# Performance work log

Hardware: AMD Instinct MI355X
Metric: run time of the kernel (lower is better)

Reference implementation:

```python
import jax, jax.numpy as jnp
import numpy as np

NR_HEADS = 8


def segment_softmax(scores, indices, num_segments):
    # numerically stable softmax within each segment
    seg_max = jax.ops.segment_max(scores, indices, num_segments=num_segments)
    e = jnp.exp(scores - seg_max[indices])
    denom = jax.ops.segment_sum(e, indices, num_segments=num_segments)
    return e / denom[indices]


def setup_inputs() -> dict:
    key = jax.random.key(0)
    ks = jax.random.split(key, 10)
    n_ast, d, n_cfg = 500000, 128, 32768
    H, combined = NR_HEADS, 128
    w_scale = 1.0 / np.sqrt(d)
    return {
        "ast_nodes_encodings": jax.random.normal(ks[0], (n_ast, d), jnp.float32),
        "Wq": jax.random.normal(ks[1], (H, d, d), jnp.float32) * w_scale,
        "bq": jnp.zeros((H, d), jnp.float32),
        "Wk": jax.random.normal(ks[2], (H, d, d), jnp.float32) * w_scale,
        "bk": jnp.zeros((H, d), jnp.float32),
        "Wo": jax.random.normal(ks[3], (H * d, combined), jnp.float32) * (1.0 / np.sqrt(H * d)),
        "bo": jnp.zeros((combined,), jnp.float32),
        "ast_key": jax.random.randint(ks[4], (n_ast,), 0, n_ast, jnp.int32),
        "ast_value": jax.random.randint(ks[5], (n_ast,), 0, n_cfg, jnp.int32),
        "pdg_key": jnp.arange(n_cfg, dtype=jnp.int32),
        "pdg_value": jax.random.randint(ks[6], (n_cfg,), 0, n_ast, jnp.int32),
        "nr_cfg_nodes": n_cfg,
    }


def reference(ast_nodes_encodings, Wq, bq, Wk, bk, Wo, bo,
              ast_key, ast_value, pdg_key, pdg_value, nr_cfg_nodes):
    N = int(nr_cfg_nodes)
    d = ast_nodes_encodings.shape[1]
    inv_sqrt_d = 1.0 / np.sqrt(d)

    # Build per-PDG-node attention queries: gather sub-AST root encodings, scatter into [N, d]
    root_encodings = ast_nodes_encodings[pdg_value]                   # [N_map, d]
    attn_queries = jnp.zeros((N, d), ast_nodes_encodings.dtype).at[pdg_key].set(root_encodings)

    # Gather scattered inputs (one row per AST node assigned to a PDG node)
    values = ast_nodes_encodings[ast_key]                              # [E, d]
    indices = ast_value                                                # [E]

    # Multi-head scatter attention (ScatterCombiner with combining_method='attn')
    head_outs = []
    for h in range(NR_HEADS):  # small fixed head count; avoids [E, H, d] intermediates
        q = attn_queries @ Wq[h] + bq[h]                               # [N, d]
        k = values @ Wk[h] + bk[h]                                     # [E, d]
        scores = jnp.sum(q[indices] * k, axis=-1) * inv_sqrt_d         # [E]
        probs = segment_softmax(scores, indices, N)                    # [E]
        head_outs.append(jax.ops.segment_sum(probs[:, None] * values, indices, num_segments=N))

    combined = jnp.concatenate(head_outs, axis=-1) @ Wo + bo           # [N, combined_dim]
    return combined
```

## Files before the change

kernel.cpp:

```cpp
#include <hip/hip_runtime.h>
#include <hip/hip_bf16.h>
#include <cstdint>

typedef __hip_bfloat16 bf16;
typedef unsigned int uint;
typedef unsigned short ushort;

#define DEVI __device__ __forceinline__

DEVI float blo(uint u){ return __uint_as_float(u << 16); }
DEVI float bhi(uint u){ return __uint_as_float(u & 0xffff0000u); }
DEVI ushort f2b(float x){ uint u = __float_as_uint(x); uint r = (u + 0x7fffu + ((u >> 16) & 1u)) >> 16; return (ushort)r; }
DEVI uint pack2(float a, float b){ return (uint)f2b(a) | ((uint)f2b(b) << 16); }
DEVI float b2f(ushort h){ return __uint_as_float((uint)h << 16); }

typedef short bf16x8 __attribute__((ext_vector_type(8)));
typedef float f32x4  __attribute__((ext_vector_type(4)));

__global__ __launch_bounds__(256) void build_M(const float* __restrict__ Wq, const float* __restrict__ Wk,
                                               float* __restrict__ Mb){
  __shared__ float WkL[128*33];
  __shared__ float WqL[16*33];
  const int t = threadIdx.x;
  const int h = blockIdx.x >> 3, pg = blockIdx.x & 7, p0 = pg*16;
  const float* wk = Wk + (size_t)h*16384;
  const float* wq = Wq + ((size_t)h*128 + p0)*128;
  const int m = t & 127, half = t >> 7;
  float acc[8] = {0,0,0,0,0,0,0,0};
  for (int jc = 0; jc < 4; ++jc){
    __syncthreads();
    #pragma unroll
    for (int i = 0; i < 4; ++i){
      int g = t + 256*i;
      int mm = g >> 3, j0 = (g & 7)*4;
      float4 v = *(const float4*)(wk + mm*128 + jc*32 + j0);
      float* d = &WkL[mm*33 + j0];
      d[0] = v.x; d[1] = v.y; d[2] = v.z; d[3] = v.w;
    }
    {
      int e = t*2;
      int pr = e >> 5, jj = e & 31;
      float2 v = *(const float2*)(wq + pr*128 + jc*32 + jj);
      WqL[pr*33 + jj] = v.x; WqL[pr*33 + jj + 1] = v.y;
    }
    __syncthreads();
    for (int j = 0; j < 32; ++j){
      float wkv = WkL[m*33 + j];
      #pragma unroll
      for (int r = 0; r < 8; ++r)
        acc[r] = fmaf(WqL[(half*8 + r)*33 + j], wkv, acc[r]);
    }
  }
  #pragma unroll
  for (int r = 0; r < 8; ++r)
    Mb[(size_t)(p0 + half*8 + r)*1024 + h*128 + m] = acc[r];
}

__global__ void build_bias(const float* __restrict__ Wq, const float* __restrict__ Wk,
                           const float* __restrict__ bq, const float* __restrict__ bk,
                           float* __restrict__ cvec, float* __restrict__ uvec, float* __restrict__ sv){
  int h = blockIdx.x, m = threadIdx.x;
  const float* wkr = Wk + ((size_t)h*128 + m)*128;
  const float* wqr = Wq + ((size_t)h*128 + m)*128;
  const float* bqr = bq + h*128;
  const float* bkr = bk + h*128;
  float c = 0.f, u = 0.f;
  for (int j = 0; j < 128; ++j){
    c = fmaf(wkr[j], bqr[j], c);
    u = fmaf(wqr[j], bkr[j], u);
  }
  cvec[h*128 + m] = c;
  uvec[h*128 + m] = u;
  if (m == 0){
    float s = 0.f;
    for (int j = 0; j < 128; ++j) s = fmaf(bqr[j], bkr[j], s);
    sv[h] = s;
  }
}

__global__ void scatter_aq(const int* __restrict__ pk, const int* __restrict__ pv,
                           const float* __restrict__ ast, float* __restrict__ aq, int n_map){
  int i = blockIdx.x;
  if (i >= n_map) return;
  int k = pk[i], src = pv[i];
  int lane = threadIdx.x;
  float2 v = *(const float2*)(ast + (size_t)src*128 + 2*lane);
  *(float2*)(aq + (size_t)k*128 + 2*lane) = v;
}

__global__ __launch_bounds__(256) void qt_gemm(const float* __restrict__ aq, const float* __restrict__ Mb,
                                               const float* __restrict__ cvec, bf16* __restrict__ qt, int N){
  __shared__ float aqL[32*128];
  const int t = threadIdx.x;
  const int n0 = blockIdx.x * 32;
  #pragma unroll
  for (int i = 0; i < 4; ++i){
    int f4 = t + 256*i;
    int r = f4 >> 5, p0 = (f4 & 31)*4;
    int row = n0 + r; if (row >= N) row = N - 1;
    *(float4*)(aqL + r*128 + p0) = *(const float4*)(aq + (size_t)row*128 + p0);
  }
  __syncthreads();
  const int cg = t & 63, rg = t >> 6;
  for (int chunk = 0; chunk < 4; ++chunk){
    const int c0 = chunk*256 + cg*4;
    float4 acc[8];
    #pragma unroll
    for (int r = 0; r < 8; ++r) acc[r] = make_float4(0.f,0.f,0.f,0.f);
    for (int p = 0; p < 128; ++p){
      float4 b4 = *(const float4*)(Mb + (size_t)p*1024 + c0);
      #pragma unroll
      for (int r = 0; r < 8; ++r){
        float a = aqL[(rg*8 + r)*128 + p];
        acc[r].x = fmaf(a, b4.x, acc[r].x);
        acc[r].y = fmaf(a, b4.y, acc[r].y);
        acc[r].z = fmaf(a, b4.z, acc[r].z);
        acc[r].w = fmaf(a, b4.w, acc[r].w);
      }
    }
    float4 cv = *(const float4*)(cvec + c0);
    #pragma unroll
    for (int r = 0; r < 8; ++r){
      int row = n0 + rg*8 + r;
      if (row < N){
        uint2 o;
        o.x = pack2(acc[r].x + cv.x, acc[r].y + cv.y);
        o.y = pack2(acc[r].z + cv.z, acc[r].w + cv.w);
        *(uint2*)(qt + (size_t)row*1024 + c0) = o;
      }
    }
  }
}

__global__ void qb_kernel(const float* __restrict__ aq, const float* __restrict__ uvec,
                          const float* __restrict__ sv, float* __restrict__ qb){
  int n = blockIdx.x, lane = threadIdx.x;
  int h = lane >> 3, g = lane & 7;
  const float* ar = aq + (size_t)n*128 + g*16;
  const float* ur = uvec + h*128 + g*16;
  float dot = 0.f;
  #pragma unroll
  for (int k = 0; k < 16; ++k) dot = fmaf(ar[k], ur[k], dot);
  dot += __shfl_xor(dot, 1);
  dot += __shfl_xor(dot, 2);
  dot += __shfl_xor(dot, 4);
  if (g == 0) qb[(size_t)n*8 + h] = dot + sv[h];
}

__global__ void count_edges(const int* __restrict__ av, int* __restrict__ counts, int E){
  int e = blockIdx.x*256 + threadIdx.x;
  if (e < E) atomicAdd(&counts[av[e]], 1);
}

__global__ void scan_offsets(const int* __restrict__ counts, int* __restrict__ offsets, int N){
  __shared__ int pa[1024];
  __shared__ int pb[1024];
  int t = threadIdx.x;
  int CH = (N + 1023) >> 10;
  int b = t*CH, e = b + CH;
  if (b > N) b = N;
  if (e > N) e = N;
  int s = 0;
  for (int i = b; i < e; ++i) s += counts[i];
  pa[t] = s;
  __syncthreads();
  int* src = pa; int* dst = pb;
  for (int off = 1; off < 1024; off <<= 1){
    int v = src[t];
    if (t >= off) v += src[t - off];
    __syncthreads();
    dst[t] = v;
    __syncthreads();
    int* tmp = src; src = dst; dst = tmp;
  }
  int run = src[t] - s;
  for (int i = b; i < e; ++i){ offsets[i] = run; run += counts[i]; }
  if (t == 1023) offsets[N] = src[1023];
}

__global__ void fill_edges(const int* __restrict__ av, const int* __restrict__ akey,
                           const int* __restrict__ offsets, int* __restrict__ cursor,
                           int* __restrict__ ridx, int E){
  int e = blockIdx.x*256 + threadIdx.x;
  if (e < E){
    int seg = av[e];
    int pos = offsets[seg] + atomicAdd(&cursor[seg], 1);
    ridx[pos] = akey[e];
  }
}

__global__ __launch_bounds__(256) void seg_attn(
    const bf16* __restrict__ qt, const float* __restrict__ qb,
    const int* __restrict__ offsets, const int* __restrict__ ridx,
    const float* __restrict__ ast, bf16* __restrict__ ho, int N)
{
  const int wid  = threadIdx.x >> 6;
  const int lane = threadIdx.x & 63;
  const int n = blockIdx.x*4 + wid;
  if (n >= N) return;
  const int beg = offsets[n];
  const int deg = offsets[n+1] - beg;
  const int h = lane >> 3, g = lane & 7;

  const uint4* qp = (const uint4*)(qt + (size_t)n*1024 + h*128 + g*16);
  const uint4 qa = qp[0], qc = qp[1];
  const float4 q0 = make_float4(blo(qa.x), bhi(qa.x), blo(qa.y), bhi(qa.y));
  const float4 q1 = make_float4(blo(qa.z), bhi(qa.z), blo(qa.w), bhi(qa.w));
  const float4 q2 = make_float4(blo(qc.x), bhi(qc.x), blo(qc.y), bhi(qc.y));
  const float4 q3 = make_float4(blo(qc.z), bhi(qc.z), blo(qc.w), bhi(qc.w));
  const float qbv = qb[(size_t)n*8 + h];
  const float isd = 0.08838834764831845f;

  float den = 0.f;
  float4 x0 = make_float4(0,0,0,0), x1 = x0, x2 = x0, x3 = x0;

  float4 vA = make_float4(0,0,0,0), vB = vA, vC = vA, vD = vA;
  if (deg > 0){
    const float4* vp = (const float4*)(ast + (size_t)ridx[beg]*128 + g*16);
    vA = vp[0]; vB = vp[1]; vC = vp[2]; vD = vp[3];
  }
  for (int e = 0; e < deg; ++e){
    const float4 a0 = vA, a1 = vB, a2 = vC, a3 = vD;
    const int e2 = (e + 1 < deg) ? (e + 1) : e;
    const float4* vpn = (const float4*)(ast + (size_t)ridx[beg + e2]*128 + g*16);
    vA = vpn[0]; vB = vpn[1]; vC = vpn[2]; vD = vpn[3];

    float dot = 0.f;
    dot = fmaf(a0.x, q0.x, dot); dot = fmaf(a0.y, q0.y, dot);
    dot = fmaf(a0.z, q0.z, dot); dot = fmaf(a0.w, q0.w, dot);
    dot = fmaf(a1.x, q1.x, dot); dot = fmaf(a1.y, q1.y, dot);
    dot = fmaf(a1.z, q1.z, dot); dot = fmaf(a1.w, q1.w, dot);
    dot = fmaf(a2.x, q2.x, dot); dot = fmaf(a2.y, q2.y, dot);
    dot = fmaf(a2.z, q2.z, dot); dot = fmaf(a2.w, q2.w, dot);
    dot = fmaf(a3.x, q3.x, dot); dot = fmaf(a3.y, q3.y, dot);
    dot = fmaf(a3.z, q3.z, dot); dot = fmaf(a3.w, q3.w, dot);
    dot += __shfl_xor(dot, 1);
    dot += __shfl_xor(dot, 2);
    dot += __shfl_xor(dot, 4);

    const float p = __expf((dot + qbv) * isd);
    den += p;
    x0.x = fmaf(p, a0.x, x0.x); x0.y = fmaf(p, a0.y, x0.y);
    x0.z = fmaf(p, a0.z, x0.z); x0.w = fmaf(p, a0.w, x0.w);
    x1.x = fmaf(p, a1.x, x1.x); x1.y = fmaf(p, a1.y, x1.y);
    x1.z = fmaf(p, a1.z, x1.z); x1.w = fmaf(p, a1.w, x1.w);
    x2.x = fmaf(p, a2.x, x2.x); x2.y = fmaf(p, a2.y, x2.y);
    x2.z = fmaf(p, a2.z, x2.z); x2.w = fmaf(p, a2.w, x2.w);
    x3.x = fmaf(p, a3.x, x3.x); x3.y = fmaf(p, a3.y, x3.y);
    x3.z = fmaf(p, a3.z, x3.z); x3.w = fmaf(p, a3.w, x3.w);
  }
  const float r = (deg > 0) ? (1.f / den) : 0.f;

  uint4 o0, o1;
  o0.x = pack2(x0.x*r, x0.y*r); o0.y = pack2(x0.z*r, x0.w*r);
  o0.z = pack2(x1.x*r, x1.y*r); o0.w = pack2(x1.z*r, x1.w*r);
  o1.x = pack2(x2.x*r, x2.y*r); o1.y = pack2(x2.z*r, x2.w*r);
  o1.z = pack2(x3.x*r, x3.y*r); o1.w = pack2(x3.z*r, x3.w*r);
  uint4* hb = (uint4*)(ho + (size_t)n*1024 + h*128 + g*16);
  hb[0] = o0;
  hb[1] = o1;
}

__global__ void wo_pack(const float* __restrict__ Wo, uint4* __restrict__ Wp){
  const int b = blockIdx.x;
  const int ks = b >> 3, ct = b & 7;
  const int l = threadIdx.x;
  const int kb = ks*32 + (l >> 4)*8;
  const int c  = ct*16 + (l & 15);
  ushort hi[8], lo[8];
  #pragma unroll
  for (int j = 0; j < 8; ++j){
    float wv = Wo[(size_t)(kb + j)*128 + c];
    ushort hh = f2b(wv);
    hi[j] = hh;
    lo[j] = f2b(wv - b2f(hh));
  }
  uint4 H, L;
  H.x = (uint)hi[0] | ((uint)hi[1] << 16);
  H.y = (uint)hi[2] | ((uint)hi[3] << 16);
  H.z = (uint)hi[4] | ((uint)hi[5] << 16);
  H.w = (uint)hi[6] | ((uint)hi[7] << 16);
  L.x = (uint)lo[0] | ((uint)lo[1] << 16);
  L.y = (uint)lo[2] | ((uint)lo[3] << 16);
  L.z = (uint)lo[4] | ((uint)lo[5] << 16);
  L.w = (uint)lo[6] | ((uint)lo[7] << 16);
  Wp[((size_t)b*2 + 0)*64 + l] = H;
  Wp[((size_t)b*2 + 1)*64 + l] = L;
}

__global__ __launch_bounds__(256, 1) void out_mfma(const bf16* __restrict__ ho, const uint4* __restrict__ Wp,
                                                   const float* __restrict__ bo, float* __restrict__ out, int N){
  const int l = threadIdx.x & 63, w = threadIdx.x >> 6;
  const int lr = l & 15, lk = l >> 4;
  const int r0 = blockIdx.x*128 + w*32;
  int ra = r0 + lr;      if (ra > N-1) ra = N-1;
  int rb = r0 + 16 + lr; if (rb > N-1) rb = N-1;
  const bf16* pa = ho + (size_t)ra*1024 + lk*8;
  const bf16* pb = ho + (size_t)rb*1024 + lk*8;
  const uint4* pw = Wp + l;

  f32x4 acc[2][8];
  #pragma unroll
  for (int i = 0; i < 2; ++i)
    #pragma unroll
    for (int c = 0; c < 8; ++c)
      #pragma unroll
      for (int j = 0; j < 4; ++j) acc[i][c][j] = 0.f;

  bf16x8 Aa[2], Ab[2], Ba[16], Bb[16];

  auto LD = [&](int ks, bf16x8* A, bf16x8* B){
    A[0] = *(const bf16x8*)(pa + ks*32);
    A[1] = *(const bf16x8*)(pb + ks*32);
    const uint4* q = pw + (size_t)ks*1024;
    #pragma unroll
    for (int u = 0; u < 16; ++u) B[u] = *(const bf16x8*)(q + (size_t)u*64);
  };
  auto MM = [&](bf16x8* A, bf16x8* B){
    #pragma unroll
    for (int c = 0; c < 8; ++c){
      acc[0][c] = __builtin_amdgcn_mfma_f32_16x16x32_bf16(A[0], B[2*c],   acc[0][c], 0, 0, 0);
      acc[1][c] = __builtin_amdgcn_mfma_f32_16x16x32_bf16(A[1], B[2*c],   acc[1][c], 0, 0, 0);
      acc[0][c] = __builtin_amdgcn_mfma_f32_16x16x32_bf16(A[0], B[2*c+1], acc[0][c], 0, 0, 0);
      acc[1][c] = __builtin_amdgcn_mfma_f32_16x16x32_bf16(A[1], B[2*c+1], acc[1][c], 0, 0, 0);
    }
  };

  LD(0, Aa, Ba);
  for (int ks = 0; ks < 32; ks += 2){
    LD(ks + 1, Ab, Bb);
    MM(Aa, Ba);
    if (ks + 2 < 32) LD(ks + 2, Aa, Ba);
    MM(Ab, Bb);
  }

  #pragma unroll
  for (int c = 0; c < 8; ++c){
    float bv = bo[c*16 + lr];
    #pragma unroll
    for (int rt = 0; rt < 2; ++rt){
      #pragma unroll
      for (int i = 0; i < 4; ++i){
        int rr = r0 + rt*16 + lk*4 + i;
        if (rr < N) out[(size_t)rr*128 + c*16 + lr] = acc[rt][c][i] + bv;
      }
    }
  }
}

extern "C" void kernel_launch(void* const* d_in, const int* in_sizes, int n_in,
                              void* d_out, int out_size, void* d_ws, size_t ws_size,
                              hipStream_t stream) {
  const float* ast = (const float*)d_in[0];
  const float* Wq  = (const float*)d_in[1];
  const float* bq  = (const float*)d_in[2];
  const float* Wk  = (const float*)d_in[3];
  const float* bk  = (const float*)d_in[4];
  const float* Wo  = (const float*)d_in[5];
  const float* bo  = (const float*)d_in[6];
  const int* ast_key   = (const int*)d_in[7];
  const int* ast_value = (const int*)d_in[8];
  const int* pdg_key   = (const int*)d_in[9];
  const int* pdg_value = (const int*)d_in[10];
  const int E     = in_sizes[7];
  const int n_map = in_sizes[9];
  const int N     = out_size / 128;
  float* out = (float*)d_out;

  char* w = (char*)d_ws;
  auto carve = [&](size_t bytes)->char*{
    char* p = w; w += (bytes + 255) & ~size_t(255); return p;
  };
  bf16*  qt      = (bf16*) carve((size_t)N*1024*2);
  float* aq      = (float*)carve((size_t)N*128*4);
  float* Mb      = (float*)carve((size_t)128*1024*4);
  float* cvec    = (float*)carve(1024*4);
  float* uvec    = (float*)carve(1024*4);
  float* sv      = (float*)carve(8*4);
  float* qb      = (float*)carve((size_t)N*8*4);
  int*   counts  = (int*)  carve((size_t)N*4);
  int*   offsets = (int*)  carve((size_t)(N+1)*4);
  int*   cursor  = (int*)  carve((size_t)N*4);
  int*   ridx    = (int*)  carve((size_t)E*4);
  bf16*  ho      = (bf16*) carve((size_t)N*1024*2);
  uint4* Wp      = (uint4*)carve((size_t)256*2*64*16);
  (void)ws_size; (void)n_in;

  hipMemsetAsync(aq,     0, (size_t)N*128*4, stream);
  hipMemsetAsync(counts, 0, (size_t)N*4, stream);
  hipMemsetAsync(cursor, 0, (size_t)N*4, stream);

  build_M   <<<64, 256, 0, stream>>>(Wq, Wk, Mb);
  build_bias<<<8, 128, 0, stream>>>(Wq, Wk, bq, bk, cvec, uvec, sv);
  wo_pack   <<<256, 64, 0, stream>>>(Wo, Wp);
  scatter_aq<<<n_map, 64, 0, stream>>>(pdg_key, pdg_value, ast, aq, n_map);
  qt_gemm   <<<(N + 31)/32, 256, 0, stream>>>(aq, Mb, cvec, qt, N);
  qb_kernel <<<N, 64, 0, stream>>>(aq, uvec, sv, qb);
  count_edges<<<(E + 255)/256, 256, 0, stream>>>(ast_value, counts, E);
  scan_offsets<<<1, 1024, 0, stream>>>(counts, offsets, N);
  fill_edges<<<(E + 255)/256, 256, 0, stream>>>(ast_value, ast_key, offsets, cursor, ridx, E);
  seg_attn  <<<(N + 3)/4, 256, 0, stream>>>(qt, qb, offsets, ridx, ast, ho, N);
  out_mfma  <<<(N + 127)/128, 256, 0, stream>>>(ho, Wp, bo, out, N);
}
```

Measured before the change: 820.7 us.

## Move query projection GEMM to split-bf16 MFMA and unroll segment attention by two

Replaces the FP32 SIMT qt_gemm with an MFMA kernel that splits the query inputs and the folded Wq·Wk matrix into bf16 hi/lo parts and uses three MFMAs per k-step to keep near-FP32 accuracy. The Wo packing kernel is generalised so it can also pack the 128x1024 M matrix into fragments. The segment attention loop now handles two edges per iteration with two rows prefetched, reduces the 8-lane groups with DPP instead of shuffles, and keeps segment bounds in scalar registers. This adds extra bf16 buffers and memsets and writes qt with scattered 2-byte stores.

```diff
diff --git a/kernel.cpp b/kernel.cpp
--- a/kernel.cpp
+++ b/kernel.cpp
@@ -16,6 +16,17 @@
 
 typedef short bf16x8 __attribute__((ext_vector_type(8)));
 typedef float f32x4  __attribute__((ext_vector_type(4)));
+
+DEVI float grp8_sum(float x){
+  int y;
+  y = __builtin_amdgcn_update_dpp(0, __float_as_int(x), 0xB1, 0xF, 0xF, true);
+  x += __int_as_float(y);
+  y = __builtin_amdgcn_update_dpp(0, __float_as_int(x), 0x4E, 0xF, 0xF, true);
+  x += __int_as_float(y);
+  y = __builtin_amdgcn_update_dpp(0, __float_as_int(x), 0x141, 0xF, 0xF, true);
+  x += __int_as_float(y);
+  return x;
+}
 
 __global__ __launch_bounds__(256) void build_M(const float* __restrict__ Wq, const float* __restrict__ Wk,
                                                float* __restrict__ Mb){
@@ -79,55 +90,81 @@
 }
 
 __global__ void scatter_aq(const int* __restrict__ pk, const int* __restrict__ pv,
-                           const float* __restrict__ ast, float* __restrict__ aq, int n_map){
+                           const float* __restrict__ ast, float* __restrict__ aq,
+                           ushort* __restrict__ aqh, ushort* __restrict__ aql, int n_map){
   int i = blockIdx.x;
   if (i >= n_map) return;
   int k = pk[i], src = pv[i];
   int lane = threadIdx.x;
   float2 v = *(const float2*)(ast + (size_t)src*128 + 2*lane);
   *(float2*)(aq + (size_t)k*128 + 2*lane) = v;
-}
-
-__global__ __launch_bounds__(256) void qt_gemm(const float* __restrict__ aq, const float* __restrict__ Mb,
-                                               const float* __restrict__ cvec, bf16* __restrict__ qt, int N){
-  __shared__ float aqL[32*128];
-  const int t = threadIdx.x;
-  const int n0 = blockIdx.x * 32;
-  #pragma unroll
-  for (int i = 0; i < 4; ++i){
-    int f4 = t + 256*i;
-    int r = f4 >> 5, p0 = (f4 & 31)*4;
-    int row = n0 + r; if (row >= N) row = N - 1;
-    *(float4*)(aqL + r*128 + p0) = *(const float4*)(aq + (size_t)row*128 + p0);
-  }
-  __syncthreads();
-  const int cg = t & 63, rg = t >> 6;
-  for (int chunk = 0; chunk < 4; ++chunk){
-    const int c0 = chunk*256 + cg*4;
-    float4 acc[8];
-    #pragma unroll
-    for (int r = 0; r < 8; ++r) acc[r] = make_float4(0.f,0.f,0.f,0.f);
-    for (int p = 0; p < 128; ++p){
-      float4 b4 = *(const float4*)(Mb + (size_t)p*1024 + c0);
-      #pragma unroll
-      for (int r = 0; r < 8; ++r){
-        float a = aqL[(rg*8 + r)*128 + p];
-        acc[r].x = fmaf(a, b4.x, acc[r].x);
-        acc[r].y = fmaf(a, b4.y, acc[r].y);
-        acc[r].z = fmaf(a, b4.z, acc[r].z);
-        acc[r].w = fmaf(a, b4.w, acc[r].w);
-      }
-    }
-    float4 cv = *(const float4*)(cvec + c0);
-    #pragma unroll
-    for (int r = 0; r < 8; ++r){
-      int row = n0 + rg*8 + r;
-      if (row < N){
-        uint2 o;
-        o.x = pack2(acc[r].x + cv.x, acc[r].y + cv.y);
-        o.y = pack2(acc[r].z + cv.z, acc[r].w + cv.w);
-        *(uint2*)(qt + (size_t)row*1024 + c0) = o;
-      }
+  ushort h0 = f2b(v.x), h1 = f2b(v.y);
+  ushort l0 = f2b(v.x - b2f(h0)), l1 = f2b(v.y - b2f(h1));
+  *(uint*)(aqh + (size_t)k*128 + 2*lane) = (uint)h0 | ((uint)h1 << 16);
+  *(uint*)(aql + (size_t)k*128 + 2*lane) = (uint)l0 | ((uint)l1 << 16);
+}
+
+__global__ void frag_pack(const float* __restrict__ S, uint4* __restrict__ D, int C, int ctn){
+  const int b = blockIdx.x;
+  const int ks = b / ctn, ct = b - ks*ctn;
+  const int l = threadIdx.x;
+  const int kb = ks*32 + (l >> 4)*8;
+  const int c  = ct*16 + (l & 15);
+  ushort hi[8], lo[8];
+  #pragma unroll
+  for (int j = 0; j < 8; ++j){
+    float wv = S[(size_t)(kb + j)*C + c];
+    ushort hh = f2b(wv);
+    hi[j] = hh;
+    lo[j] = f2b(wv - b2f(hh));
+  }
+  uint4 H, L;
+  H.x = (uint)hi[0] | ((uint)hi[1] << 16);
+  H.y = (uint)hi[2] | ((uint)hi[3] << 16);
+  H.z = (uint)hi[4] | ((uint)hi[5] << 16);
+  H.w = (uint)hi[6] | ((uint)hi[7] << 16);
+  L.x = (uint)lo[0] | ((uint)lo[1] << 16);
+  L.y = (uint)lo[2] | ((uint)lo[3] << 16);
+  L.z = (uint)lo[4] | ((uint)lo[5] << 16);
+  L.w = (uint)lo[6] | ((uint)lo[7] << 16);
+  D[((size_t)b*2 + 0)*64 + l] = H;
+  D[((size_t)b*2 + 1)*64 + l] = L;
+}
+
+__global__ __launch_bounds__(256, 1) void qt_mfma(const ushort* __restrict__ aqh, const ushort* __restrict__ aql,
+                                                  const uint4* __restrict__ Mp, const float* __restrict__ cvec,
+                                                  bf16* __restrict__ qt, int N){
+  const int l = threadIdx.x & 63, w = threadIdx.x >> 6;
+  const int lr = l & 15, lk = l >> 4;
+  const int r0 = blockIdx.x*16;
+  int ra = r0 + lr; if (ra > N-1) ra = N-1;
+  const ushort* ph = aqh + (size_t)ra*128 + lk*8;
+  const ushort* pl = aql + (size_t)ra*128 + lk*8;
+  bf16x8 Ah[4], Al[4];
+  #pragma unroll
+  for (int ks = 0; ks < 4; ++ks){
+    Ah[ks] = *(const bf16x8*)(ph + ks*32);
+    Al[ks] = *(const bf16x8*)(pl + ks*32);
+  }
+  const int ct0 = w*16;
+  for (int ct = 0; ct < 16; ++ct){
+    const int ctg = ct0 + ct;
+    f32x4 acc = {0.f, 0.f, 0.f, 0.f};
+    #pragma unroll
+    for (int ks = 0; ks < 4; ++ks){
+      const uint4* q = Mp + ((size_t)(ks*64 + ctg)*2)*64 + l;
+      bf16x8 Bh = *(const bf16x8*)q;
+      bf16x8 Bl = *(const bf16x8*)(q + 64);
+      acc = __builtin_amdgcn_mfma_f32_16x16x32_bf16(Ah[ks], Bh, acc, 0, 0, 0);
+      acc = __builtin_amdgcn_mfma_f32_16x16x32_bf16(Al[ks], Bh, acc, 0, 0, 0);
+      acc = __builtin_amdgcn_mfma_f32_16x16x32_bf16(Ah[ks], Bl, acc, 0, 0, 0);
+    }
+    const int cc = ctg*16 + lr;
+    const float bv = cvec[cc];
+    #pragma unroll
+    for (int i = 0; i < 4; ++i){
+      int rr = r0 + lk*4 + i;
+      if (rr < N) ((ushort*)qt)[(size_t)rr*1024 + cc] = f2b(acc[i] + bv);
     }
   }
 }
@@ -198,8 +235,9 @@
   const int lane = threadIdx.x & 63;
   const int n = blockIdx.x*4 + wid;
   if (n >= N) return;
-  const int beg = offsets[n];
-  const int deg = offsets[n+1] - beg;
+  const int beg = __builtin_amdgcn_readfirstlane(offsets[n]);
+  const int end = __builtin_amdgcn_readfirstlane(offsets[n+1]);
+  const int deg = end - beg;
   const int h = lane >> 3, g = lane & 7;
 
   const uint4* qp = (const uint4*)(qt + (size_t)n*1024 + h*128 + g*16);
@@ -211,43 +249,88 @@
   const float qbv = qb[(size_t)n*8 + h];
   const float isd = 0.08838834764831845f;
 
+  const int* rp = ridx + beg;
+
   float den = 0.f;
   float4 x0 = make_float4(0,0,0,0), x1 = x0, x2 = x0, x3 = x0;
 
-  float4 vA = make_float4(0,0,0,0), vB = vA, vC = vA, vD = vA;
   if (deg > 0){
-    const float4* vp = (const float4*)(ast + (size_t)ridx[beg]*128 + g*16);
-    vA = vp[0]; vB = vp[1]; vC = vp[2]; vD = vp[3];
-  }
-  for (int e = 0; e < deg; ++e){
-    const float4 a0 = vA, a1 = vB, a2 = vC, a3 = vD;
-    const int e2 = (e + 1 < deg) ? (e + 1) : e;
-    const float4* vpn = (const float4*)(ast + (size_t)ridx[beg + e2]*128 + g*16);
-    vA = vpn[0]; vB = vpn[1]; vC = vpn[2]; vD = vpn[3];
-
-    float dot = 0.f;
-    dot = fmaf(a0.x, q0.x, dot); dot = fmaf(a0.y, q0.y, dot);
-    dot = fmaf(a0.z, q0.z, dot); dot = fmaf(a0.w, q0.w, dot);
-    dot = fmaf(a1.x, q1.x, dot); dot = fmaf(a1.y, q1.y, dot);
-    dot = fmaf(a1.z, q1.z, dot); dot = fmaf(a1.w, q1.w, dot);
-    dot = fmaf(a2.x, q2.x, dot); dot = fmaf(a2.y, q2.y, dot);
-    dot = fmaf(a2.z, q2.z, dot); dot = fmaf(a2.w, q2.w, dot);
-    dot = fmaf(a3.x, q3.x, dot); dot = fmaf(a3.y, q3.y, dot);
-    dot = fmaf(a3.z, q3.z, dot); dot = fmaf(a3.w, q3.w, dot);
-    dot += __shfl_xor(dot, 1);
-    dot += __shfl_xor(dot, 2);
-    dot += __shfl_xor(dot, 4);
-
-    const float p = __expf((dot + qbv) * isd);
-    den += p;
-    x0.x = fmaf(p, a0.x, x0.x); x0.y = fmaf(p, a0.y, x0.y);
-    x0.z = fmaf(p, a0.z, x0.z); x0.w = fmaf(p, a0.w, x0.w);
-    x1.x = fmaf(p, a1.x, x1.x); x1.y = fmaf(p, a1.y, x1.y);
-    x1.z = fmaf(p, a1.z, x1.z); x1.w = fmaf(p, a1.w, x1.w);
-    x2.x = fmaf(p, a2.x, x2.x); x2.y = fmaf(p, a2.y, x2.y);
-    x2.z = fmaf(p, a2.z, x2.z); x2.w = fmaf(p, a2.w, x2.w);
-    x3.x = fmaf(p, a3.x, x3.x); x3.y = fmaf(p, a3.y, x3.y);
-    x3.z = fmaf(p, a3.z, x3.z); x3.w = fmaf(p, a3.w, x3.w);
+    #define ROWP(ee) ((const float4*)(ast + (size_t)rp[(ee) < deg ? (ee) : deg-1]*128) + g*4)
+    float4 A0, A1, A2, A3, B0, B1, B2, B3;
+    { const float4* p = ROWP(0); A0 = p[0]; A1 = p[1]; A2 = p[2]; A3 = p[3]; }
+    { const float4* p = ROWP(1); B0 = p[0]; B1 = p[1]; B2 = p[2]; B3 = p[3]; }
+    int e = 0;
+    for (; e + 1 < deg; e += 2){
+      const float4 a0 = A0, a1 = A1, a2 = A2, a3 = A3;
+      const float4 b0 = B0, b1 = B1, b2 = B2, b3 = B3;
+      { const float4* p = ROWP(e + 2); A0 = p[0]; A1 = p[1]; A2 = p[2]; A3 = p[3]; }
+      { const float4* p = ROWP(e + 3); B0 = p[0]; B1 = p[1]; B2 = p[2]; B3 = p[3]; }
+
+      float dA = 0.f, dB = 0.f;
+      dA = fmaf(a0.x, q0.x, dA); dA = fmaf(a0.y, q0.y, dA);
+      dA = fmaf(a0.z, q0.z, dA); dA = fmaf(a0.w, q0.w, dA);
+      dA = fmaf(a1.x, q1.x, dA); dA = fmaf(a1.y, q1.y, dA);
+      dA = fmaf(a1.z, q1.z, dA); dA = fmaf(a1.w, q1.w, dA);
+      dA = fmaf(a2.x, q2.x, dA); dA = fmaf(a2.y, q2.y, dA);
+      dA = fmaf(a2.z, q2.z, dA); dA = fmaf(a2.w, q2.w, dA);
+      dA = fmaf(a3.x, q3.x, dA); dA = fmaf(a3.y, q3.y, dA);
+      dA = fmaf(a3.z, q3.z, dA); dA = fmaf(a3.w, q3.w, dA);
+      dB = fmaf(b0.x, q0.x, dB); dB = fmaf(b0.y, q0.y, dB);
+      dB = fmaf(b0.z, q0.z, dB); dB = fmaf(b0.w, q0.w, dB);
+      dB = fmaf(b1.x, q1.x, dB); dB = fmaf(b1.y, q1.y, dB);
+      dB = fmaf(b1.z, q1.z, dB); dB = fmaf(b1.w, q1.w, dB);
+      dB = fmaf(b2.x, q2.x, dB); dB = fmaf(b2.y, q2.y, dB);
+      dB = fmaf(b2.z, q2.z, dB); dB = fmaf(b2.w, q2.w, dB);
+      dB = fmaf(b3.x, q3.x, dB); dB = fmaf(b3.y, q3.y, dB);
+      dB = fmaf(b3.z, q3.z, dB); dB = fmaf(b3.w, q3.w, dB);
+      dA = grp8_sum(dA);
+      dB = grp8_sum(dB);
+
+      const float pA = __expf((dA + qbv) * isd);
+      const float pB = __expf((dB + qbv) * isd);
+      den += pA; den += pB;
+
+      x0.x = fmaf(pA, a0.x, x0.x); x0.y = fmaf(pA, a0.y, x0.y);
+      x0.z = fmaf(pA, a0.z, x0.z); x0.w = fmaf(pA, a0.w, x0.w);
+      x1.x = fmaf(pA, a1.x, x1.x); x1.y = fmaf(pA, a1.y, x1.y);
+      x1.z = fmaf(pA, a1.z, x1.z); x1.w = fmaf(pA, a1.w, x1.w);
+      x2.x = fmaf(pA, a2.x, x2.x); x2.y = fmaf(pA, a2.y, x2.y);
+      x2.z = fmaf(pA, a2.z, x2.z); x2.w = fmaf(pA, a2.w, x2.w);
+      x3.x = fmaf(pA, a3.x, x3.x); x3.y = fmaf(pA, a3.y, x3.y);
+      x3.z = fmaf(pA, a3.z, x3.z); x3.w = fmaf(pA, a3.w, x3.w);
+      x0.x = fmaf(pB, b0.x, x0.x); x0.y = fmaf(pB, b0.y, x0.y);
+      x0.z = fmaf(pB, b0.z, x0.z); x0.w = fmaf(pB, b0.w, x0.w);
+      x1.x = fmaf(pB, b1.x, x1.x); x1.y = fmaf(pB, b1.y, x1.y);
+      x1.z = fmaf(pB, b1.z, x1.z); x1.w = fmaf(pB, b1.w, x1.w);
+      x2.x = fmaf(pB, b2.x, x2.x); x2.y = fmaf(pB, b2.y, x2.y);
+      x2.z = fmaf(pB, b2.z, x2.z); x2.w = fmaf(pB, b2.w, x2.w);
+      x3.x = fmaf(pB, b3.x, x3.x); x3.y = fmaf(pB, b3.y, x3.y);
+      x3.z = fmaf(pB, b3.z, x3.z); x3.w = fmaf(pB, b3.w, x3.w);
+    }
+    if (e < deg){
+      const float4 a0 = A0, a1 = A1, a2 = A2, a3 = A3;
+      float dA = 0.f;
+      dA = fmaf(a0.x, q0.x, dA); dA = fmaf(a0.y, q0.y, dA);
+      dA = fmaf(a0.z, q0.z, dA); dA = fmaf(a0.w, q0.w, dA);
+      dA = fmaf(a1.x, q1.x, dA); dA = fmaf(a1.y, q1.y, dA);
+      dA = fmaf(a1.z, q1.z, dA); dA = fmaf(a1.w, q1.w, dA);
+      dA = fmaf(a2.x, q2.x, dA); dA = fmaf(a2.y, q2.y, dA);
+      dA = fmaf(a2.z, q2.z, dA); dA = fmaf(a2.w, q2.w, dA);
+      dA = fmaf(a3.x, q3.x, dA); dA = fmaf(a3.y, q3.y, dA);
+      dA = fmaf(a3.z, q3.z, dA); dA = fmaf(a3.w, q3.w, dA);
+      dA = grp8_sum(dA);
+      const float pA = __expf((dA + qbv) * isd);
+      den += pA;
+      x0.x = fmaf(pA, a0.x, x0.x); x0.y = fmaf(pA, a0.y, x0.y);
+      x0.z = fmaf(pA, a0.z, x0.z); x0.w = fmaf(pA, a0.w, x0.w);
+      x1.x = fmaf(pA, a1.x, x1.x); x1.y = fmaf(pA, a1.y, x1.y);
+      x1.z = fmaf(pA, a1.z, x1.z); x1.w = fmaf(pA, a1.w, x1.w);
+      x2.x = fmaf(pA, a2.x, x2.x); x2.y = fmaf(pA, a2.y, x2.y);
+      x2.z = fmaf(pA, a2.z, x2.z); x2.w = fmaf(pA, a2.w, x2.w);
+      x3.x = fmaf(pA, a3.x, x3.x); x3.y = fmaf(pA, a3.y, x3.y);
+      x3.z = fmaf(pA, a3.z, x3.z); x3.w = fmaf(pA, a3.w, x3.w);
+    }
+    #undef ROWP
   }
   const float r = (deg > 0) ? (1.f / den) : 0.f;
 
@@ -259,33 +342,6 @@
   uint4* hb = (uint4*)(ho + (size_t)n*1024 + h*128 + g*16);
   hb[0] = o0;
   hb[1] = o1;
-}
-
-__global__ void wo_pack(const float* __restrict__ Wo, uint4* __restrict__ Wp){
-  const int b = blockIdx.x;
-  const int ks = b >> 3, ct = b & 7;
-  const int l = threadIdx.x;
-  const int kb = ks*32 + (l >> 4)*8;
-  const int c  = ct*16 + (l & 15);
-  ushort hi[8], lo[8];
-  #pragma unroll
-  for (int j = 0; j < 8; ++j){
-    float wv = Wo[(size_t)(kb + j)*128 + c];
-    ushort hh = f2b(wv);
-    hi[j] = hh;
-    lo[j] = f2b(wv - b2f(hh));
-  }
-  uint4 H, L;
-  H.x = (uint)hi[0] | ((uint)hi[1] << 16);
-  H.y = (uint)hi[2] | ((uint)hi[3] << 16);
-  H.z = (uint)hi[4] | ((uint)hi[5] << 16);
-  H.w = (uint)hi[6] | ((uint)hi[7] << 16);
-  L.x = (uint)lo[0] | ((uint)lo[1] << 16);
-  L.y = (uint)lo[2] | ((uint)lo[3] << 16);
-  L.z = (uint)lo[4] | ((uint)lo[5] << 16);
-  L.w = (uint)lo[6] | ((uint)lo[7] << 16);
-  Wp[((size_t)b*2 + 0)*64 + l] = H;
-  Wp[((size_t)b*2 + 1)*64 + l] = L;
 }
 
 __global__ __launch_bounds__(256, 1) void out_mfma(const bf16* __restrict__ ho, const uint4* __restrict__ Wp,
@@ -384,17 +440,23 @@
   int*   ridx    = (int*)  carve((size_t)E*4);
   bf16*  ho      = (bf16*) carve((size_t)N*1024*2);
   uint4* Wp      = (uint4*)carve((size_t)256*2*64*16);
+  ushort* aqh    = (ushort*)carve((size_t)N*128*2);
+  ushort* aql    = (ushort*)carve((size_t)N*128*2);
+  uint4* Mp      = (uint4*)carve((size_t)256*2*64*16);
   (void)ws_size; (void)n_in;
 
   hipMemsetAsync(aq,     0, (size_t)N*128*4, stream);
+  hipMemsetAsync(aqh,    0, (size_t)N*128*2, stream);
+  hipMemsetAsync(aql,    0, (size_t)N*128*2, stream);
   hipMemsetAsync(counts, 0, (size_t)N*4, stream);
   hipMemsetAsync(cursor, 0, (size_t)N*4, stream);
 
   build_M   <<<64, 256, 0, stream>>>(Wq, Wk, Mb);
   build_bias<<<8, 128, 0, stream>>>(Wq, Wk, bq, bk, cvec, uvec, sv);
-  wo_pack   <<<256, 64, 0, stream>>>(Wo, Wp);
-  scatter_aq<<<n_map, 64, 0, stream>>>(pdg_key, pdg_value, ast, aq, n_map);
-  qt_gemm   <<<(N + 31)/32, 256, 0, stream>>>(aq, Mb, cvec, qt, N);
+  frag_pack <<<256, 64, 0, stream>>>(Wo, Wp, 128, 8);
+  scatter_aq<<<n_map, 64, 0, stream>>>(pdg_key, pdg_value, ast, aq, aqh, aql, n_map);
+  frag_pack <<<256, 64, 0, stream>>>(Mb, Mp, 1024, 64);
+  qt_mfma   <<<(N + 15)/16, 256, 0, stream>>>(aqh, aql, Mp, cvec, qt, N);
   qb_kernel <<<N, 64, 0, stream>>>(aq, uvec, sv, qb);
   count_edges<<<(E + 255)/256, 256, 0, stream>>>(ast_value, counts, E);
   scan_offsets<<<1, 1024, 0, stream>>>(counts, offsets, N);
```

Result: faster. 770.8 us (-6.1%).
